# Kernel tuning notes

Hardware: AMD Instinct MI355X
Metric: run time of the kernel (lower is better)

The kernel has to match this reference:

```python
import jax, jax.numpy as jnp
import numpy as np

HIDDEN = 128
IN = 28
OUT = 28


def _uniform(key, shape, fan_in):
    bound = 1.0 / np.sqrt(fan_in)
    return jax.random.uniform(key, shape, jnp.float32, -bound, bound)


def setup_inputs() -> dict:
    key = jax.random.key(0)
    ks = jax.random.split(key, 8)
    B, T = 4096, 256
    x = jax.random.normal(ks[0], (B, T, IN), jnp.float32)
    hidden = jnp.zeros((B, HIDDEN), jnp.float32)
    # torch nn.Linear default init: U(-1/sqrt(fan_in), 1/sqrt(fan_in))
    W_ih = _uniform(ks[1], (HIDDEN, IN), IN)
    b_ih = _uniform(ks[2], (HIDDEN,), IN)
    W_hh = _uniform(ks[3], (HIDDEN, HIDDEN), HIDDEN)
    b_hh = _uniform(ks[4], (HIDDEN,), HIDDEN)
    W_ho = _uniform(ks[5], (OUT * OUT, HIDDEN), HIDDEN)
    b_ho = _uniform(ks[6], (OUT * OUT,), HIDDEN)
    return {"x": x, "hidden": hidden, "W_ih": W_ih, "b_ih": b_ih,
            "W_hh": W_hh, "b_hh": b_hh, "W_ho": W_ho, "b_ho": b_ho}


def reference(x, hidden, W_ih, b_ih, W_hh, b_hh, W_ho, b_ho):
    # x: [B, T, IN]; hidden: [B, HIDDEN]
    def step(h, x_t):
        h = jax.nn.relu(x_t @ W_ih.T + b_ih + h @ W_hh.T + b_hh)
        return h, None

    # scan over time (leading axis) — equivalent to the python loop,
    # and only the final hidden feeds the output projection (the torch
    # code overwrites `output` every step, so only the last one matters).
    h_final, _ = jax.lax.scan(step, hidden, jnp.swapaxes(x, 0, 1))
    out = (h_final @ W_ho.T + b_ho).reshape(-1, OUT, OUT)  # [B, 28, 28]
    return out, h_final
```

## Files before the change

kernel.cpp:

```cpp
#include <hip/hip_runtime.h>
#include <hip/hip_bf16.h>

#define B_TOT   4096
#define T_STEPS 256
#define IN_D    28
#define HID     128
#define OUT_D   784
#define BM      16

typedef __bf16 bf16x8 __attribute__((ext_vector_type(8)));
typedef __bf16 bf16x4 __attribute__((ext_vector_type(4)));
typedef float  f32x4  __attribute__((ext_vector_type(4)));
typedef float  f32x2  __attribute__((ext_vector_type(2)));

__device__ __forceinline__ float bf2f(__bf16 b) {
    unsigned short s = __builtin_bit_cast(unsigned short, b);
    unsigned int u = ((unsigned int)s) << 16;
    return __builtin_bit_cast(float, u);
}
__device__ __forceinline__ unsigned short f2bfbits(float f) {
    unsigned int u = __builtin_bit_cast(unsigned int, f);
    u += 0x7fffu + ((u >> 16) & 1u);
    return (unsigned short)(u >> 16);
}

__device__ __forceinline__ int hswz(int row, int byteInRow) {
    return row * 256 + (byteInRow ^ ((row & 7) << 4));
}

__global__ __launch_bounds__(256) void rnn_fused(
    const float* __restrict__ x,
    const float* __restrict__ h0,
    const float* __restrict__ W_ih,
    const float* __restrict__ b_ih,
    const float* __restrict__ W_hh,
    const float* __restrict__ b_hh,
    const float* __restrict__ W_ho,
    const float* __restrict__ b_ho,
    float* __restrict__ out)
{
    __shared__ __align__(16) unsigned char Hb[2][BM * 256];
    __shared__ __align__(16) unsigned char Xs[8 * 1024];

    const int tid  = threadIdx.x;
    const int lane = tid & 63;
    const int wv   = tid >> 6;
    const int ln15 = lane & 15;
    const int lg   = lane >> 4;
    const int b0   = blockIdx.x * BM;

    const int nt0 = wv * 32;
    bf16x8 bw[2][4];
    #pragma unroll
    for (int ti = 0; ti < 2; ++ti) {
        int n = nt0 + ti * 16 + ln15;
        #pragma unroll
        for (int kc = 0; kc < 4; ++kc) {
            const float* p = W_hh + n * HID + kc * 32 + lg * 8;
            bf16x8 v;
            #pragma unroll
            for (int e = 0; e < 8; ++e) v[e] = (__bf16)p[e];
            bw[ti][kc] = v;
        }
    }
    const __bf16 bzero = (__bf16)0.0f;
    bf16x8 bxf[2];
    #pragma unroll
    for (int ti = 0; ti < 2; ++ti) {
        int n = nt0 + ti * 16 + ln15;
        bf16x8 v;
        #pragma unroll
        for (int e = 0; e < 8; ++e) {
            int k = lg * 8 + e;
            v[e] = (k < IN_D) ? (__bf16)W_ih[n * IN_D + k] : bzero;
        }
        bxf[ti] = v;
    }
    f32x4 bias4[2];
    #pragma unroll
    for (int ti = 0; ti < 2; ++ti) {
        int n = nt0 + ti * 16 + 4 * lg;
        f32x4 bi = *(const f32x4*)(b_ih + n);
        f32x4 bh = *(const f32x4*)(b_hh + n);
        bias4[ti] = bi + bh;
    }

    {
        int row = tid >> 4, cg = tid & 15;
        const float* p = h0 + (size_t)(b0 + row) * HID + cg * 8;
        bf16x8 hv;
        #pragma unroll
        for (int e = 0; e < 8; ++e) hv[e] = (__bf16)p[e];
        *(bf16x8*)(&Hb[0][hswz(row, cg * 16)]) = hv;
    }
    {
        int slot = tid >> 5, idx = tid & 31, row = idx >> 1, d = idx & 1;
        *(unsigned int*)(&Xs[slot * 1024 + row * 64 + 56 + d * 4]) = 0u;
    }
    const int xrow = tid / 14, xpair = tid % 14;
    const bool xthr = (tid < 224);
    const float* xbase = x + (size_t)(b0 + xrow) * T_STEPS * IN_D + xpair * 2;
    if (xthr) {
        #pragma unroll
        for (int s = 0; s < 4; ++s) {
            f32x2 v = *(const f32x2*)(xbase + (size_t)s * IN_D);
            unsigned int pk = ((unsigned int)f2bfbits(v[1]) << 16) | f2bfbits(v[0]);
            *(unsigned int*)(&Xs[s * 1024 + xrow * 64 + xpair * 4]) = pk;
        }
    }
    f32x2 sx0 = {0.f, 0.f}, sx1 = sx0, sx2 = sx0, sx3 = sx0;
    __syncthreads();

#define STEP(T, STGL, STGW)                                                     \
    {                                                                           \
        const int rb = (T) & 1;                                                 \
        STGL                                                                    \
        bf16x8 ax  = *(const bf16x8*)(&Xs[((T) & 7) * 1024 + ln15 * 64 + lg * 16]); \
        bf16x8 ah0 = *(const bf16x8*)(&Hb[rb][hswz(ln15,   0 + lg * 16)]);      \
        bf16x8 ah1 = *(const bf16x8*)(&Hb[rb][hswz(ln15,  64 + lg * 16)]);      \
        bf16x8 ah2 = *(const bf16x8*)(&Hb[rb][hswz(ln15, 128 + lg * 16)]);      \
        bf16x8 ah3 = *(const bf16x8*)(&Hb[rb][hswz(ln15, 192 + lg * 16)]);      \
        f32x4 a0 = __builtin_amdgcn_mfma_f32_16x16x32_bf16(bxf[0], ax, bias4[0], 0, 0, 0); \
        f32x4 a1 = __builtin_amdgcn_mfma_f32_16x16x32_bf16(bxf[1], ax, bias4[1], 0, 0, 0); \
        f32x4 zz = {0.f, 0.f, 0.f, 0.f};                                        \
        a0 = __builtin_amdgcn_mfma_f32_16x16x32_bf16(bw[0][0], ah0, a0, 0, 0, 0); \
        a1 = __builtin_amdgcn_mfma_f32_16x16x32_bf16(bw[1][0], ah0, a1, 0, 0, 0); \
        f32x4 c0 = __builtin_amdgcn_mfma_f32_16x16x32_bf16(bw[0][1], ah1, zz, 0, 0, 0); \
        f32x4 c1 = __builtin_amdgcn_mfma_f32_16x16x32_bf16(bw[1][1], ah1, zz, 0, 0, 0); \
        a0 = __builtin_amdgcn_mfma_f32_16x16x32_bf16(bw[0][2], ah2, a0, 0, 0, 0); \
        a1 = __builtin_amdgcn_mfma_f32_16x16x32_bf16(bw[1][2], ah2, a1, 0, 0, 0); \
        c0 = __builtin_amdgcn_mfma_f32_16x16x32_bf16(bw[0][3], ah3, c0, 0, 0, 0); \
        c1 = __builtin_amdgcn_mfma_f32_16x16x32_bf16(bw[1][3], ah3, c1, 0, 0, 0); \
        _Pragma("unroll")                                                       \
        for (int ti = 0; ti < 2; ++ti) {                                        \
            f32x4 s = ti ? (a1 + c1) : (a0 + c0);                               \
            bf16x4 w;                                                           \
            _Pragma("unroll")                                                   \
            for (int r = 0; r < 4; ++r) {                                       \
                float v = s[r];                                                 \
                w[r] = (__bf16)(v > 0.f ? v : 0.f);                             \
            }                                                                   \
            *(bf16x4*)(&Hb[rb ^ 1][hswz(ln15, nt0 * 2 + ti * 32 + lg * 8)]) = w; \
        }                                                                       \
        STGW                                                                    \
        __syncthreads();                                                        \
    }

#define STG_LOAD(T)                                                             \
        if (((T) + 4 < T_STEPS) && xthr) {                                      \
            sx0 = *(const f32x2*)(xbase + (size_t)((T) + 4) * IN_D);            \
            sx1 = *(const f32x2*)(xbase + (size_t)((T) + 5) * IN_D);            \
            sx2 = *(const f32x2*)(xbase + (size_t)((T) + 6) * IN_D);            \
            sx3 = *(const f32x2*)(xbase + (size_t)((T) + 7) * IN_D);            \
        }
#define STG_WRITE(T)                                                            \
        if (((T) + 4 < T_STEPS) && xthr) {                                      \
            unsigned int p0 = ((unsigned int)f2bfbits(sx0[1]) << 16) | f2bfbits(sx0[0]); \
            unsigned int p1 = ((unsigned int)f2bfbits(sx1[1]) << 16) | f2bfbits(sx1[0]); \
            unsigned int p2 = ((unsigned int)f2bfbits(sx2[1]) << 16) | f2bfbits(sx2[0]); \
            unsigned int p3 = ((unsigned int)f2bfbits(sx3[1]) << 16) | f2bfbits(sx3[0]); \
            *(unsigned int*)(&Xs[(((T) + 4) & 7) * 1024 + xrow * 64 + xpair * 4]) = p0; \
            *(unsigned int*)(&Xs[(((T) + 5) & 7) * 1024 + xrow * 64 + xpair * 4]) = p1; \
            *(unsigned int*)(&Xs[(((T) + 6) & 7) * 1024 + xrow * 64 + xpair * 4]) = p2; \
            *(unsigned int*)(&Xs[(((T) + 7) & 7) * 1024 + xrow * 64 + xpair * 4]) = p3; \
        }

    for (int t = 0; t < T_STEPS; t += 8) {
        STEP(t + 0, STG_LOAD(t + 0), STG_WRITE(t + 0))
        STEP(t + 1, , )
        STEP(t + 2, , )
        STEP(t + 3, , )
        STEP(t + 4, STG_LOAD(t + 4), STG_WRITE(t + 4))
        STEP(t + 5, , )
        STEP(t + 6, , )
        STEP(t + 7, , )
    }
#undef STEP
#undef STG_LOAD
#undef STG_WRITE

    {
        int row = tid >> 4, cg = tid & 15;
        bf16x8 hv = *(const bf16x8*)(&Hb[0][hswz(row, cg * 16)]);
        float* po = out + (size_t)B_TOT * OUT_D + (size_t)(b0 + row) * HID + cg * 8;
        #pragma unroll
        for (int e = 0; e < 8; ++e) po[e] = bf2f(hv[e]);
    }
    bf16x8 af[4];
    #pragma unroll
    for (int kc = 0; kc < 4; ++kc)
        af[kc] = *(const bf16x8*)(&Hb[0][hswz(ln15, kc * 64 + lg * 16)]);

    for (int nt = wv; nt < 49; nt += 4) {
        f32x4 acc = *(const f32x4*)(b_ho + nt * 16 + 4 * lg);
        #pragma unroll
        for (int kc = 0; kc < 4; ++kc) {
            const float* p = W_ho + (nt * 16 + ln15) * HID + kc * 32 + lg * 8;
            bf16x8 bfrag;
            #pragma unroll
            for (int e = 0; e < 8; ++e) bfrag[e] = (__bf16)p[e];
            acc = __builtin_amdgcn_mfma_f32_16x16x32_bf16(bfrag, af[kc], acc, 0, 0, 0);
        }
        *(f32x4*)(out + (size_t)(b0 + ln15) * OUT_D + nt * 16 + 4 * lg) = acc;
    }
}

extern "C" void kernel_launch(void* const* d_in, const int* in_sizes, int n_in,
                              void* d_out, int out_size, void* d_ws, size_t ws_size,
                              hipStream_t stream) {
    const float* x    = (const float*)d_in[0];
    const float* h0   = (const float*)d_in[1];
    const float* W_ih = (const float*)d_in[2];
    const float* b_ih = (const float*)d_in[3];
    const float* W_hh = (const float*)d_in[4];
    const float* b_hh = (const float*)d_in[5];
    const float* W_ho = (const float*)d_in[6];
    const float* b_ho = (const float*)d_in[7];
    rnn_fused<<<B_TOT / BM, 256, 0, stream>>>(x, h0, W_ih, b_ih, W_hh, b_hh,
                                              W_ho, b_ho, (float*)d_out);
}
```

Before: 104.6 us.

## Split hidden dimension across eight waves per block instead of four

Doubles the block size to 512 threads so each wave computes one 16-column tile of the hidden state per timestep instead of two. This shortens the per-wave MFMA dependency chain in the serial recurrence and spreads the output projection over more waves. In exchange, each per-step barrier synchronises twice as many waves, and register pressure is bounded for 512 threads.

```diff
diff --git a/kernel.cpp b/kernel.cpp
--- a/kernel.cpp
+++ b/kernel.cpp
@@ -28,7 +28,7 @@
     return row * 256 + (byteInRow ^ ((row & 7) << 4));
 }
 
-__global__ __launch_bounds__(256) void rnn_fused(
+__global__ __launch_bounds__(512) void rnn_fused(
     const float* __restrict__ x,
     const float* __restrict__ h0,
     const float* __restrict__ W_ih,
@@ -49,43 +49,35 @@
     const int lg   = lane >> 4;
     const int b0   = blockIdx.x * BM;
 
-    const int nt0 = wv * 32;
-    bf16x8 bw[2][4];
+    const int nt0 = wv * 16;
+    bf16x8 bw[4];
     #pragma unroll
-    for (int ti = 0; ti < 2; ++ti) {
-        int n = nt0 + ti * 16 + ln15;
-        #pragma unroll
-        for (int kc = 0; kc < 4; ++kc) {
-            const float* p = W_hh + n * HID + kc * 32 + lg * 8;
-            bf16x8 v;
-            #pragma unroll
-            for (int e = 0; e < 8; ++e) v[e] = (__bf16)p[e];
-            bw[ti][kc] = v;
-        }
+    for (int kc = 0; kc < 4; ++kc) {
+        const float* p = W_hh + (nt0 + ln15) * HID + kc * 32 + lg * 8;
+        bf16x8 v;
+        #pragma unroll
+        for (int e = 0; e < 8; ++e) v[e] = (__bf16)p[e];
+        bw[kc] = v;
     }
     const __bf16 bzero = (__bf16)0.0f;
-    bf16x8 bxf[2];
-    #pragma unroll
-    for (int ti = 0; ti < 2; ++ti) {
-        int n = nt0 + ti * 16 + ln15;
-        bf16x8 v;
+    bf16x8 bxf;
+    {
+        int n = nt0 + ln15;
         #pragma unroll
         for (int e = 0; e < 8; ++e) {
             int k = lg * 8 + e;
-            v[e] = (k < IN_D) ? (__bf16)W_ih[n * IN_D + k] : bzero;
-        }
-        bxf[ti] = v;
-    }
-    f32x4 bias4[2];
-    #pragma unroll
-    for (int ti = 0; ti < 2; ++ti) {
-        int n = nt0 + ti * 16 + 4 * lg;
+            bxf[e] = (k < IN_D) ? (__bf16)W_ih[n * IN_D + k] : bzero;
+        }
+    }
+    f32x4 bias4;
+    {
+        int n = nt0 + 4 * lg;
         f32x4 bi = *(const f32x4*)(b_ih + n);
         f32x4 bh = *(const f32x4*)(b_hh + n);
-        bias4[ti] = bi + bh;
-    }
-
-    {
+        bias4 = bi + bh;
+    }
+
+    if (tid < 256) {
         int row = tid >> 4, cg = tid & 15;
         const float* p = h0 + (size_t)(b0 + row) * HID + cg * 8;
         bf16x8 hv;
@@ -93,7 +85,7 @@
         for (int e = 0; e < 8; ++e) hv[e] = (__bf16)p[e];
         *(bf16x8*)(&Hb[0][hswz(row, cg * 16)]) = hv;
     }
-    {
+    if (tid < 256) {
         int slot = tid >> 5, idx = tid & 31, row = idx >> 1, d = idx & 1;
         *(unsigned int*)(&Xs[slot * 1024 + row * 64 + 56 + d * 4]) = 0u;
     }
@@ -120,28 +112,20 @@
         bf16x8 ah1 = *(const bf16x8*)(&Hb[rb][hswz(ln15,  64 + lg * 16)]);      \
         bf16x8 ah2 = *(const bf16x8*)(&Hb[rb][hswz(ln15, 128 + lg * 16)]);      \
         bf16x8 ah3 = *(const bf16x8*)(&Hb[rb][hswz(ln15, 192 + lg * 16)]);      \
-        f32x4 a0 = __builtin_amdgcn_mfma_f32_16x16x32_bf16(bxf[0], ax, bias4[0], 0, 0, 0); \
-        f32x4 a1 = __builtin_amdgcn_mfma_f32_16x16x32_bf16(bxf[1], ax, bias4[1], 0, 0, 0); \
         f32x4 zz = {0.f, 0.f, 0.f, 0.f};                                        \
-        a0 = __builtin_amdgcn_mfma_f32_16x16x32_bf16(bw[0][0], ah0, a0, 0, 0, 0); \
-        a1 = __builtin_amdgcn_mfma_f32_16x16x32_bf16(bw[1][0], ah0, a1, 0, 0, 0); \
-        f32x4 c0 = __builtin_amdgcn_mfma_f32_16x16x32_bf16(bw[0][1], ah1, zz, 0, 0, 0); \
-        f32x4 c1 = __builtin_amdgcn_mfma_f32_16x16x32_bf16(bw[1][1], ah1, zz, 0, 0, 0); \
-        a0 = __builtin_amdgcn_mfma_f32_16x16x32_bf16(bw[0][2], ah2, a0, 0, 0, 0); \
-        a1 = __builtin_amdgcn_mfma_f32_16x16x32_bf16(bw[1][2], ah2, a1, 0, 0, 0); \
-        c0 = __builtin_amdgcn_mfma_f32_16x16x32_bf16(bw[0][3], ah3, c0, 0, 0, 0); \
-        c1 = __builtin_amdgcn_mfma_f32_16x16x32_bf16(bw[1][3], ah3, c1, 0, 0, 0); \
+        f32x4 a = __builtin_amdgcn_mfma_f32_16x16x32_bf16(bxf,   ax,  bias4, 0, 0, 0); \
+        f32x4 c = __builtin_amdgcn_mfma_f32_16x16x32_bf16(bw[1], ah1, zz, 0, 0, 0); \
+        a = __builtin_amdgcn_mfma_f32_16x16x32_bf16(bw[0], ah0, a, 0, 0, 0);    \
+        c = __builtin_amdgcn_mfma_f32_16x16x32_bf16(bw[3], ah3, c, 0, 0, 0);    \
+        a = __builtin_amdgcn_mfma_f32_16x16x32_bf16(bw[2], ah2, a, 0, 0, 0);    \
+        f32x4 s = a + c;                                                        \
+        bf16x4 w;                                                               \
         _Pragma("unroll")                                                       \
-        for (int ti = 0; ti < 2; ++ti) {                                        \
-            f32x4 s = ti ? (a1 + c1) : (a0 + c0);                               \
-            bf16x4 w;                                                           \
-            _Pragma("unroll")                                                   \
-            for (int r = 0; r < 4; ++r) {                                       \
-                float v = s[r];                                                 \
-                w[r] = (__bf16)(v > 0.f ? v : 0.f);                             \
-            }                                                                   \
-            *(bf16x4*)(&Hb[rb ^ 1][hswz(ln15, nt0 * 2 + ti * 32 + lg * 8)]) = w; \
+        for (int r = 0; r < 4; ++r) {                                           \
+            float v = s[r];                                                     \
+            w[r] = (__bf16)(v > 0.f ? v : 0.f);                                 \
         }                                                                       \
+        *(bf16x4*)(&Hb[rb ^ 1][hswz(ln15, nt0 * 2 + lg * 8)]) = w;              \
         STGW                                                                    \
         __syncthreads();                                                        \
     }
@@ -179,7 +163,7 @@
 #undef STG_LOAD
 #undef STG_WRITE
 
-    {
+    if (tid < 256) {
         int row = tid >> 4, cg = tid & 15;
         bf16x8 hv = *(const bf16x8*)(&Hb[0][hswz(row, cg * 16)]);
         float* po = out + (size_t)B_TOT * OUT_D + (size_t)(b0 + row) * HID + cg * 8;
@@ -191,7 +175,7 @@
     for (int kc = 0; kc < 4; ++kc)
         af[kc] = *(const bf16x8*)(&Hb[0][hswz(ln15, kc * 64 + lg * 16)]);
 
-    for (int nt = wv; nt < 49; nt += 4) {
+    for (int nt = wv; nt < 49; nt += 8) {
         f32x4 acc = *(const f32x4*)(b_ho + nt * 16 + 4 * lg);
         #pragma unroll
         for (int kc = 0; kc < 4; ++kc) {
@@ -216,6 +200,6 @@
     const float* b_hh = (const float*)d_in[5];
     const float* W_ho = (const float*)d_in[6];
     const float* b_ho = (const float*)d_in[7];
-    rnn_fused<<<B_TOT / BM, 256, 0, stream>>>(x, h0, W_ih, b_ih, W_hh, b_hh,
+    rnn_fused<<<B_TOT / BM, 512, 0, stream>>>(x, h0, W_ih, b_ih, W_hh, b_hh,
                                               W_ho, b_ho, (float*)d_out);
 }
```

Measured after the change: 96.97 us. 7.3% less time.

## Batch input projections per 8-step block and use LDS-only barriers

Applied to the files above, without the earlier changes.

The input-projection MFMAs for eight timesteps are now computed together at the start of each 8-step block, from a fully staged 8-slot X buffer. Each recurrent step then starts its accumulation from these precomputed values, which takes one dependent MFMA off the per-step critical chain. The per-step __syncthreads is replaced by an inline s_waitcnt lgkmcnt(0) plus s_barrier, so in-flight global prefetches of x no longer stall the barrier. The X staging buffer is enlarged and swizzled like the hidden buffer, and the prefetch schedule is shifted to fill slots after they are consumed. The cost is more LDS (32KB for X) and sixteen extra live accumulator vectors, which raises register pressure.

```diff
diff --git a/kernel.cpp b/kernel.cpp
--- a/kernel.cpp
+++ b/kernel.cpp
@@ -27,6 +27,8 @@
 __device__ __forceinline__ int hswz(int row, int byteInRow) {
     return row * 256 + (byteInRow ^ ((row & 7) << 4));
 }
+
+#define BARLDS() asm volatile("s_waitcnt lgkmcnt(0)\n\ts_barrier" ::: "memory")
 
 __global__ __launch_bounds__(256) void rnn_fused(
     const float* __restrict__ x,
@@ -40,7 +42,7 @@
     float* __restrict__ out)
 {
     __shared__ __align__(16) unsigned char Hb[2][BM * 256];
-    __shared__ __align__(16) unsigned char Xs[8 * 1024];
+    __shared__ __align__(16) unsigned char Xs[8 * BM * 256];
 
     const int tid  = threadIdx.x;
     const int lane = tid & 63;
@@ -95,36 +97,65 @@
     }
     {
         int slot = tid >> 5, idx = tid & 31, row = idx >> 1, d = idx & 1;
-        *(unsigned int*)(&Xs[slot * 1024 + row * 64 + 56 + d * 4]) = 0u;
+        *(unsigned int*)(&Xs[slot * (BM * 256) + hswz(row, 56 + d * 4)]) = 0u;
     }
     const int xrow = tid / 14, xpair = tid % 14;
     const bool xthr = (tid < 224);
     const float* xbase = x + (size_t)(b0 + xrow) * T_STEPS * IN_D + xpair * 2;
     if (xthr) {
         #pragma unroll
-        for (int s = 0; s < 4; ++s) {
+        for (int s = 0; s < 8; ++s) {
             f32x2 v = *(const f32x2*)(xbase + (size_t)s * IN_D);
             unsigned int pk = ((unsigned int)f2bfbits(v[1]) << 16) | f2bfbits(v[0]);
-            *(unsigned int*)(&Xs[s * 1024 + xrow * 64 + xpair * 4]) = pk;
+            *(unsigned int*)(&Xs[s * (BM * 256) + hswz(xrow, xpair * 4)]) = pk;
         }
     }
     f32x2 sx0 = {0.f, 0.f}, sx1 = sx0, sx2 = sx0, sx3 = sx0;
     __syncthreads();
 
-#define STEP(T, STGL, STGW)                                                     \
+    f32x4 u0a, u1a, u2a, u3a, u4a, u5a, u6a, u7a;
+    f32x4 u0b, u1b, u2b, u3b, u4b, u5b, u6b, u7b;
+
+#define PRE8(T)                                                                 \
+        {                                                                       \
+            bf16x8 ax0 = *(const bf16x8*)(&Xs[0 * (BM * 256) + hswz(ln15, lg * 16)]); \
+            bf16x8 ax1 = *(const bf16x8*)(&Xs[1 * (BM * 256) + hswz(ln15, lg * 16)]); \
+            bf16x8 ax2 = *(const bf16x8*)(&Xs[2 * (BM * 256) + hswz(ln15, lg * 16)]); \
+            bf16x8 ax3 = *(const bf16x8*)(&Xs[3 * (BM * 256) + hswz(ln15, lg * 16)]); \
+            bf16x8 ax4 = *(const bf16x8*)(&Xs[4 * (BM * 256) + hswz(ln15, lg * 16)]); \
+            bf16x8 ax5 = *(const bf16x8*)(&Xs[5 * (BM * 256) + hswz(ln15, lg * 16)]); \
+            bf16x8 ax6 = *(const bf16x8*)(&Xs[6 * (BM * 256) + hswz(ln15, lg * 16)]); \
+            bf16x8 ax7 = *(const bf16x8*)(&Xs[7 * (BM * 256) + hswz(ln15, lg * 16)]); \
+            u0a = __builtin_amdgcn_mfma_f32_16x16x32_bf16(bxf[0], ax0, bias4[0], 0, 0, 0); \
+            u0b = __builtin_amdgcn_mfma_f32_16x16x32_bf16(bxf[1], ax0, bias4[1], 0, 0, 0); \
+            u1a = __builtin_amdgcn_mfma_f32_16x16x32_bf16(bxf[0], ax1, bias4[0], 0, 0, 0); \
+            u1b = __builtin_amdgcn_mfma_f32_16x16x32_bf16(bxf[1], ax1, bias4[1], 0, 0, 0); \
+            u2a = __builtin_amdgcn_mfma_f32_16x16x32_bf16(bxf[0], ax2, bias4[0], 0, 0, 0); \
+            u2b = __builtin_amdgcn_mfma_f32_16x16x32_bf16(bxf[1], ax2, bias4[1], 0, 0, 0); \
+            u3a = __builtin_amdgcn_mfma_f32_16x16x32_bf16(bxf[0], ax3, bias4[0], 0, 0, 0); \
+            u3b = __builtin_amdgcn_mfma_f32_16x16x32_bf16(bxf[1], ax3, bias4[1], 0, 0, 0); \
+            u4a = __builtin_amdgcn_mfma_f32_16x16x32_bf16(bxf[0], ax4, bias4[0], 0, 0, 0); \
+            u4b = __builtin_amdgcn_mfma_f32_16x16x32_bf16(bxf[1], ax4, bias4[1], 0, 0, 0); \
+            u5a = __builtin_amdgcn_mfma_f32_16x16x32_bf16(bxf[0], ax5, bias4[0], 0, 0, 0); \
+            u5b = __builtin_amdgcn_mfma_f32_16x16x32_bf16(bxf[1], ax5, bias4[1], 0, 0, 0); \
+            u6a = __builtin_amdgcn_mfma_f32_16x16x32_bf16(bxf[0], ax6, bias4[0], 0, 0, 0); \
+            u6b = __builtin_amdgcn_mfma_f32_16x16x32_bf16(bxf[1], ax6, bias4[1], 0, 0, 0); \
+            u7a = __builtin_amdgcn_mfma_f32_16x16x32_bf16(bxf[0], ax7, bias4[0], 0, 0, 0); \
+            u7b = __builtin_amdgcn_mfma_f32_16x16x32_bf16(bxf[1], ax7, bias4[1], 0, 0, 0); \
+        }
+
+#define STEP(T, UA, UB, PRE, STGL, STGW)                                        \
     {                                                                           \
         const int rb = (T) & 1;                                                 \
+        PRE                                                                     \
         STGL                                                                    \
-        bf16x8 ax  = *(const bf16x8*)(&Xs[((T) & 7) * 1024 + ln15 * 64 + lg * 16]); \
         bf16x8 ah0 = *(const bf16x8*)(&Hb[rb][hswz(ln15,   0 + lg * 16)]);      \
         bf16x8 ah1 = *(const bf16x8*)(&Hb[rb][hswz(ln15,  64 + lg * 16)]);      \
         bf16x8 ah2 = *(const bf16x8*)(&Hb[rb][hswz(ln15, 128 + lg * 16)]);      \
         bf16x8 ah3 = *(const bf16x8*)(&Hb[rb][hswz(ln15, 192 + lg * 16)]);      \
-        f32x4 a0 = __builtin_amdgcn_mfma_f32_16x16x32_bf16(bxf[0], ax, bias4[0], 0, 0, 0); \
-        f32x4 a1 = __builtin_amdgcn_mfma_f32_16x16x32_bf16(bxf[1], ax, bias4[1], 0, 0, 0); \
         f32x4 zz = {0.f, 0.f, 0.f, 0.f};                                        \
-        a0 = __builtin_amdgcn_mfma_f32_16x16x32_bf16(bw[0][0], ah0, a0, 0, 0, 0); \
-        a1 = __builtin_amdgcn_mfma_f32_16x16x32_bf16(bw[1][0], ah0, a1, 0, 0, 0); \
+        f32x4 a0 = __builtin_amdgcn_mfma_f32_16x16x32_bf16(bw[0][0], ah0, UA, 0, 0, 0); \
+        f32x4 a1 = __builtin_amdgcn_mfma_f32_16x16x32_bf16(bw[1][0], ah0, UB, 0, 0, 0); \
         f32x4 c0 = __builtin_amdgcn_mfma_f32_16x16x32_bf16(bw[0][1], ah1, zz, 0, 0, 0); \
         f32x4 c1 = __builtin_amdgcn_mfma_f32_16x16x32_bf16(bw[1][1], ah1, zz, 0, 0, 0); \
         a0 = __builtin_amdgcn_mfma_f32_16x16x32_bf16(bw[0][2], ah2, a0, 0, 0, 0); \
@@ -143,39 +174,40 @@
             *(bf16x4*)(&Hb[rb ^ 1][hswz(ln15, nt0 * 2 + ti * 32 + lg * 8)]) = w; \
         }                                                                       \
         STGW                                                                    \
-        __syncthreads();                                                        \
-    }
-
-#define STG_LOAD(T)                                                             \
-        if (((T) + 4 < T_STEPS) && xthr) {                                      \
-            sx0 = *(const f32x2*)(xbase + (size_t)((T) + 4) * IN_D);            \
-            sx1 = *(const f32x2*)(xbase + (size_t)((T) + 5) * IN_D);            \
-            sx2 = *(const f32x2*)(xbase + (size_t)((T) + 6) * IN_D);            \
-            sx3 = *(const f32x2*)(xbase + (size_t)((T) + 7) * IN_D);            \
-        }
-#define STG_WRITE(T)                                                            \
-        if (((T) + 4 < T_STEPS) && xthr) {                                      \
-            unsigned int p0 = ((unsigned int)f2bfbits(sx0[1]) << 16) | f2bfbits(sx0[0]); \
-            unsigned int p1 = ((unsigned int)f2bfbits(sx1[1]) << 16) | f2bfbits(sx1[0]); \
-            unsigned int p2 = ((unsigned int)f2bfbits(sx2[1]) << 16) | f2bfbits(sx2[0]); \
-            unsigned int p3 = ((unsigned int)f2bfbits(sx3[1]) << 16) | f2bfbits(sx3[0]); \
-            *(unsigned int*)(&Xs[(((T) + 4) & 7) * 1024 + xrow * 64 + xpair * 4]) = p0; \
-            *(unsigned int*)(&Xs[(((T) + 5) & 7) * 1024 + xrow * 64 + xpair * 4]) = p1; \
-            *(unsigned int*)(&Xs[(((T) + 6) & 7) * 1024 + xrow * 64 + xpair * 4]) = p2; \
-            *(unsigned int*)(&Xs[(((T) + 7) & 7) * 1024 + xrow * 64 + xpair * 4]) = p3; \
+        BARLDS();                                                               \
+    }
+
+#define STG_LOAD(TF)                                                            \
+        if (((TF) < T_STEPS) && xthr) {                                         \
+            sx0 = *(const f32x2*)(xbase + (size_t)((TF) + 0) * IN_D);           \
+            sx1 = *(const f32x2*)(xbase + (size_t)((TF) + 1) * IN_D);           \
+            sx2 = *(const f32x2*)(xbase + (size_t)((TF) + 2) * IN_D);           \
+            sx3 = *(const f32x2*)(xbase + (size_t)((TF) + 3) * IN_D);           \
+        }
+#define STG_WRITE(TF)                                                           \
+        if (((TF) < T_STEPS) && xthr) {                                         \
+            unsigned int q0 = ((unsigned int)f2bfbits(sx0[1]) << 16) | f2bfbits(sx0[0]); \
+            unsigned int q1 = ((unsigned int)f2bfbits(sx1[1]) << 16) | f2bfbits(sx1[0]); \
+            unsigned int q2 = ((unsigned int)f2bfbits(sx2[1]) << 16) | f2bfbits(sx2[0]); \
+            unsigned int q3 = ((unsigned int)f2bfbits(sx3[1]) << 16) | f2bfbits(sx3[0]); \
+            *(unsigned int*)(&Xs[(((TF) + 0) & 7) * (BM * 256) + hswz(xrow, xpair * 4)]) = q0; \
+            *(unsigned int*)(&Xs[(((TF) + 1) & 7) * (BM * 256) + hswz(xrow, xpair * 4)]) = q1; \
+            *(unsigned int*)(&Xs[(((TF) + 2) & 7) * (BM * 256) + hswz(xrow, xpair * 4)]) = q2; \
+            *(unsigned int*)(&Xs[(((TF) + 3) & 7) * (BM * 256) + hswz(xrow, xpair * 4)]) = q3; \
         }
 
     for (int t = 0; t < T_STEPS; t += 8) {
-        STEP(t + 0, STG_LOAD(t + 0), STG_WRITE(t + 0))
-        STEP(t + 1, , )
-        STEP(t + 2, , )
-        STEP(t + 3, , )
-        STEP(t + 4, STG_LOAD(t + 4), STG_WRITE(t + 4))
-        STEP(t + 5, , )
-        STEP(t + 6, , )
-        STEP(t + 7, , )
+        STEP(t + 0, u0a, u0b, PRE8(t), , )
+        STEP(t + 1, u1a, u1b, , STG_LOAD(t + 8), )
+        STEP(t + 2, u2a, u2b, , , )
+        STEP(t + 3, u3a, u3b, , , )
+        STEP(t + 4, u4a, u4b, , , STG_WRITE(t + 8))
+        STEP(t + 5, u5a, u5b, , STG_LOAD(t + 12), )
+        STEP(t + 6, u6a, u6b, , , )
+        STEP(t + 7, u7a, u7b, , , STG_WRITE(t + 12))
     }
 #undef STEP
+#undef PRE8
 #undef STG_LOAD
 #undef STG_WRITE
 
```

Result: faster. 95.38 us (-8.8%).
